# Performance work log

Measured on AMD Instinct MI355X. Metric: run time of the kernel, lower is better.

The kernel has to match this reference:

```python
import jax, jax.numpy as jnp
import numpy as np


def setup_inputs() -> dict:
    key = jax.random.key(0)
    k1, k2 = jax.random.split(key)
    B, V = 1024, 50257
    scores = jax.random.normal(k1, (B, V), dtype=jnp.float32)
    class_indices = jax.random.randint(k2, (B,), 0, V, dtype=jnp.int64 if jax.config.jax_enable_x64 else jnp.int32)
    return {"scores": scores, "class_indices": class_indices}


def reference(scores, class_indices):
    B, D = scores.shape
    code_len = int(np.ceil(np.log2(D)))  # static, from shape
    # sigmoid over raw tree scores, pad position 0 with 1.0 (identity for product)
    tree_probs = jax.nn.sigmoid(scores)
    padded = jnp.concatenate([jnp.ones((B, 1), scores.dtype), tree_probs], axis=1)  # [B, D+1]
    levels = jnp.arange(code_len, dtype=jnp.int32)            # l = 0..code_len-1
    shifts = (code_len - 1) - levels                           # bit tested at level l
    bits = (class_indices.astype(jnp.int32)[:, None] >> shifts[None, :]) & 1  # [B, L]
    cur_index = jnp.left_shift(jnp.int32(1), levels)           # cur_index at level l == 2**l
    # bit==0 -> take left prob at cur_index; bit==1 -> take right prob at cur_index+1;
    # the other side gathers the pad (index 0, prob 1.0), matching the torch code.
    left_idx = jnp.where(bits == 0, cur_index[None, :], 0)     # [B, L]
    right_idx = jnp.where(bits == 1, cur_index[None, :] + 1, 0)
    left_p = jnp.prod(jnp.take_along_axis(padded, left_idx, axis=1), axis=1)   # [B]
    right_p = jnp.prod(jnp.take_along_axis(padded, right_idx, axis=1), axis=1)  # [B]
    probs = left_p * right_p
    return jnp.sum(-jnp.log(probs)) / B
```

## Files before the change

### kernel.cpp

```cpp
#include <hip/hip_runtime.h>
#include <hip/hip_bf16.h>


__global__ __launch_bounds__(256) void hsm_gather_kernel(
    const float* __restrict__ scores,
    const int* __restrict__ cls,
    float* __restrict__ out,
    int B, int V, int code_len, float invB) {

    const int tid = threadIdx.x;
    const int lvl0 = tid & 15;
    const int rowInBlk = tid >> 4;
    const int rowsPerBlk = blockDim.x >> 4;

    float acc = 0.0f;
    for (int r = blockIdx.x * rowsPerBlk + rowInBlk; r < B;
         r += gridDim.x * rowsPerBlk) {
        const float* row = scores + (size_t)r * (size_t)V;
        const int ci = cls[r];
        for (int l = lvl0; l < code_len; l += 16) {
            const float a = row[(1 << l) - 1];
            const float b = row[(1 << l)];
            const int bit = (ci >> (code_len - 1 - l)) & 1;
            const float x = bit ? b : a;
            acc += log1pf(__expf(-fabsf(x))) + fmaxf(-x, 0.0f);
        }
    }

    #pragma unroll
    for (int off = 32; off > 0; off >>= 1)
        acc += __shfl_down(acc, off, 64);

    __shared__ float wsum[4];
    const int lane = tid & 63;
    const int wid = tid >> 6;
    if (lane == 0) wsum[wid] = acc;
    __syncthreads();

    if (tid == 0) {
        const float blocksum = wsum[0] + wsum[1] + wsum[2] + wsum[3];
        atomicAdd(out, blocksum * invB);
    }
}

extern "C" void kernel_launch(void* const* d_in, const int* in_sizes, int n_in,
                              void* d_out, int out_size, void* d_ws, size_t ws_size,
                              hipStream_t stream) {
    const float* scores = (const float*)d_in[0];
    const int* class_indices = (const int*)d_in[1];
    float* out = (float*)d_out;

    const int B = in_sizes[1];
    const int V = (int)(in_sizes[0] / (size_t)in_sizes[1]);

    int code_len = 0;
    while ((1LL << code_len) < (long long)V) ++code_len;

    hipMemsetAsync(out, 0, (size_t)out_size * sizeof(float), stream);

    const int rowsPerBlk = 16;
    const int grid = (B + rowsPerBlk - 1) / rowsPerBlk;
    hsm_gather_kernel<<<grid, 256, 0, stream>>>(scores, class_indices, out,
                                                B, V, code_len, 1.0f / (float)B);
}
```

Before: 11.98 us.

## Replace memset and atomics with cooperative kernel grid-sync reduction

Drops the separate memset launch and the per-block atomicAdd. The kernel now runs as a cooperative launch with a fixed 64 blocks, each storing a partial sum to workspace, and after a grid-wide sync block 0 reduces the partials and writes the result. This saves one launch and makes the reduction deterministic, at the cost of grid-sync overhead and cooperative-launch setup.

```diff
diff --git a/kernel.cpp b/kernel.cpp
--- a/kernel.cpp
+++ b/kernel.cpp
@@ -1,11 +1,17 @@
 #include <hip/hip_runtime.h>
 #include <hip/hip_bf16.h>
+#include <hip/hip_cooperative_groups.h>
+
+namespace cg = cooperative_groups;
 
 
-__global__ __launch_bounds__(256) void hsm_gather_kernel(
+#define NBLK 64
+
+__global__ __launch_bounds__(256) void hsm_coop_kernel(
     const float* __restrict__ scores,
     const int* __restrict__ cls,
     float* __restrict__ out,
+    float* __restrict__ partials,
     int B, int V, int code_len, float invB) {
 
     const int tid = threadIdx.x;
@@ -38,8 +44,20 @@
     __syncthreads();
 
     if (tid == 0) {
-        const float blocksum = wsum[0] + wsum[1] + wsum[2] + wsum[3];
-        atomicAdd(out, blocksum * invB);
+        const float p = wsum[0] + wsum[1] + wsum[2] + wsum[3];
+        __hip_atomic_store(&partials[blockIdx.x], p,
+                           __ATOMIC_RELEASE, __HIP_MEMORY_SCOPE_AGENT);
+    }
+
+    cg::this_grid().sync();
+
+    if (blockIdx.x == 0 && tid < NBLK) {
+        float v = __hip_atomic_load(&partials[tid],
+                                    __ATOMIC_ACQUIRE, __HIP_MEMORY_SCOPE_AGENT);
+        #pragma unroll
+        for (int off = 32; off > 0; off >>= 1)
+            v += __shfl_down(v, off, 64);
+        if (tid == 0) out[0] = v * invB;
     }
 }
 
@@ -49,17 +67,19 @@
     const float* scores = (const float*)d_in[0];
     const int* class_indices = (const int*)d_in[1];
     float* out = (float*)d_out;
+    float* partials = (float*)d_ws;
 
-    const int B = in_sizes[1];
-    const int V = (int)(in_sizes[0] / (size_t)in_sizes[1]);
+    int B = in_sizes[1];
+    int V = (int)(in_sizes[0] / (size_t)in_sizes[1]);
 
     int code_len = 0;
     while ((1LL << code_len) < (long long)V) ++code_len;
 
-    hipMemsetAsync(out, 0, (size_t)out_size * sizeof(float), stream);
+    float invB = 1.0f / (float)B;
 
-    const int rowsPerBlk = 16;
-    const int grid = (B + rowsPerBlk - 1) / rowsPerBlk;
-    hsm_gather_kernel<<<grid, 256, 0, stream>>>(scores, class_indices, out,
-                                                B, V, code_len, 1.0f / (float)B);
+    void* args[] = { (void*)&scores, (void*)&class_indices, (void*)&out,
+                     (void*)&partials, (void*)&B, (void*)&V,
+                     (void*)&code_len, (void*)&invB };
+    hipLaunchCooperativeKernel((void*)hsm_coop_kernel,
+                               dim3(NBLK), dim3(256), args, 0, stream);
 }
```

Result: slower. 30.80 us (+157.0%).
